# Performance work log

Measured on AMD Instinct MI355X. Metric: run time of the kernel, lower is better.

The kernel has to match this reference:

```python
import jax, jax.numpy as jnp
import numpy as np

N, D, B = 500000, 128, 2048

def setup_inputs() -> dict:
    key = jax.random.key(0)
    ks = jax.random.split(key, 7)
    x = jax.random.normal(ks[0], (N, D), dtype=jnp.float32)
    batch = jnp.sort(jax.random.randint(ks[1], (N,), 0, B)).astype(jnp.int64)
    s = 1.0 / np.sqrt(D)
    Wm = jax.random.uniform(ks[2], (D, D), jnp.float32, -s, s)  # xavier-ish
    fc1_w = jax.random.uniform(ks[3], (D // 4, D), jnp.float32, -s, s)
    fc1_b = jnp.zeros((D // 4,), jnp.float32)
    fc2_w = jax.random.uniform(ks[4], (D, D // 4), jnp.float32, -1/np.sqrt(D//4), 1/np.sqrt(D//4))
    fc2_b = jnp.zeros((D,), jnp.float32)
    return {"x": x, "batch": batch, "size": B, "Wm": Wm,
            "fc1_w": fc1_w, "fc1_b": fc1_b, "fc2_w": fc2_w, "fc2_b": fc2_b}

def reference(x, batch, size, Wm, fc1_w, fc1_b, fc2_w, fc2_b):
    batch = batch.astype(jnp.int32)
    # fc: Linear -> ReLU -> Linear -> Tanh
    attention = jnp.tanh(jax.nn.relu(x @ fc1_w.T + fc1_b) @ fc2_w.T + fc2_b)
    x2 = attention * x + x  # [N, D]
    # scatter_mean over graphs
    sums = jax.ops.segment_sum(x2, batch, num_segments=size)  # [B, D]
    cnt = jax.ops.segment_sum(jnp.ones((x2.shape[0],), x2.dtype), batch, num_segments=size)
    mean = sums / jnp.maximum(cnt, 1.0)[:, None]
    transformed_global = jnp.tanh(mean @ Wm)  # [B, D]
    coefs = jax.nn.sigmoid(jnp.sum(x2 * transformed_global[batch], axis=1))  # [N]
    weighted = coefs[:, None] * x2
    return jax.ops.segment_sum(weighted, batch, num_segments=size)  # [B, D]
```

## Files before the change

### kernel.cpp

```cpp
#include <hip/hip_runtime.h>
#include <math.h>

#define D 128
#define BLOCKS_A 768
#define BLOCKS_C 1536
#define THREADS 256

typedef short s8v __attribute__((ext_vector_type(8)));
typedef float f4v __attribute__((ext_vector_type(4)));

__device__ __forceinline__ float fast_tanh(float z) {
    float e = __expf(2.f * z);
    return 1.f - 2.f / (e + 1.f);
}
__device__ __forceinline__ unsigned cvt_pk_bf16(float lo, float hi) {
    unsigned r;
    asm("v_cvt_pk_bf16_f32 %0, %1, %2" : "=v"(r) : "v"(lo), "v"(hi));
    return r;
}
__device__ __forceinline__ s8v pack8(float4 w0, float4 w1) {
    union { unsigned u[4]; s8v v; } r;
    r.u[0] = cvt_pk_bf16(w0.x, w0.y);
    r.u[1] = cvt_pk_bf16(w0.z, w0.w);
    r.u[2] = cvt_pk_bf16(w1.x, w1.y);
    r.u[3] = cvt_pk_bf16(w1.z, w1.w);
    return r.v;
}

#define EPI0(RG_)                                                             \
    {                                                                         \
        int r = R + quad * 4 + RG_;                                           \
        int seg = batch[r];                                                   \
        const float* xrow = x + (size_t)r * 128 + m15;                        \
        float yv[8];                                                          \
        _Pragma("unroll")                                                     \
        for (int t = 0; t < 8; ++t) {                                         \
            float z = af[t][RG_] + b2l[t];                                    \
            yv[t] = xrow[16 * t] * (1.f + fast_tanh(z));                      \
        }                                                                     \
        union { unsigned u[4]; uint4 q; } pk;                                 \
        pk.u[0] = cvt_pk_bf16(yv[0], yv[1]);                                  \
        pk.u[1] = cvt_pk_bf16(yv[2], yv[3]);                                  \
        pk.u[2] = cvt_pk_bf16(yv[4], yv[5]);                                  \
        pk.u[3] = cvt_pk_bf16(yv[6], yv[7]);                                  \
        ((uint4*)x2s)[(size_t)b * 256 + RG_ * 64 + lane] = pk.q;              \
        if (seg != cur) {                                                     \
            if (cur >= 0) {                                                   \
                _Pragma("unroll")                                             \
                for (int t = 0; t < 8; ++t)                                   \
                    atomicAdd(&sums[cur * 128 + m15 + 16 * t], acc[t]);       \
                if (m15 == 0) atomicAdd(&cnt[cur], acnt);                     \
            }                                                                 \
            cur = seg;                                                        \
            _Pragma("unroll")                                                 \
            for (int t = 0; t < 8; ++t) acc[t] = yv[t];                       \
            acnt = 1.f;                                                       \
        } else {                                                              \
            _Pragma("unroll")                                                 \
            for (int t = 0; t < 8; ++t) acc[t] += yv[t];                      \
            acnt += 1.f;                                                      \
        }                                                                     \
    }

__global__ __launch_bounds__(THREADS, 3) void phaseA(
    const float* __restrict__ x, const int* __restrict__ batch,
    const float* __restrict__ fc1_w, const float* __restrict__ fc1_b,
    const float* __restrict__ fc2_w, const float* __restrict__ fc2_b,
    float* __restrict__ sums, float* __restrict__ cnt,
    unsigned short* __restrict__ x2s, int N)
{
    __shared__ s8v wB1[2][4][64];
    __shared__ s8v wB2[8][64];
    __shared__ float hbuf[4][16 * 36];

    const int lane = threadIdx.x & 63;
    const int wv = threadIdx.x >> 6;
    const int m15 = lane & 15;
    const int quad = lane >> 4;

    if (wv == 0) {
        #pragma unroll
        for (int t = 0; t < 2; ++t)
            #pragma unroll
            for (int kc = 0; kc < 4; ++kc) {
                const float* p = fc1_w + (16 * t + m15) * 128 + kc * 32 + quad * 8;
                wB1[t][kc][lane] = pack8(*(const float4*)p, *(const float4*)(p + 4));
            }
        #pragma unroll
        for (int t = 0; t < 8; ++t) {
            const float* p = fc2_w + (16 * t + m15) * 32 + quad * 8;
            wB2[t][lane] = pack8(*(const float4*)p, *(const float4*)(p + 4));
        }
    }
    float b1l[2], b2l[8];
    #pragma unroll
    for (int t = 0; t < 2; ++t) b1l[t] = fc1_b[m15 + 16 * t];
    #pragma unroll
    for (int t = 0; t < 8; ++t) b2l[t] = fc2_b[m15 + 16 * t];
    __syncthreads();

    const int total16 = N >> 4;
    const int nw = BLOCKS_A * 4;
    const int gw = blockIdx.x * 4 + wv;
    const int base = total16 / nw, rem = total16 % nw;
    const int b0 = gw * base + (gw < rem ? gw : rem);
    const int b1e = b0 + base + (gw < rem ? 1 : 0);

    float* hw = hbuf[wv];

    float acc[8];
    #pragma unroll
    for (int t = 0; t < 8; ++t) acc[t] = 0.f;
    int cur = -1;
    float acnt = 0.f;
    const f4v z4 = {0.f, 0.f, 0.f, 0.f};

    float4 F[8];
    if (b0 < b1e) {
        const float* xp = x + (size_t)(b0 << 4) * D + m15 * 128 + quad * 8;
        #pragma unroll
        for (int kc = 0; kc < 4; ++kc) {
            F[2 * kc]     = *(const float4*)(xp + kc * 32);
            F[2 * kc + 1] = *(const float4*)(xp + kc * 32 + 4);
        }
    }

    for (int b = b0; b < b1e; ++b) {
        const int R = b << 4;
        s8v ax[4];
        #pragma unroll
        for (int kc = 0; kc < 4; ++kc)
            ax[kc] = pack8(F[2 * kc], F[2 * kc + 1]);
        if (b + 1 < b1e) {
            const float* xp = x + (size_t)((b + 1) << 4) * D + m15 * 128 + quad * 8;
            #pragma unroll
            for (int kc = 0; kc < 4; ++kc) {
                F[2 * kc]     = *(const float4*)(xp + kc * 32);
                F[2 * kc + 1] = *(const float4*)(xp + kc * 32 + 4);
            }
        }
        f4v accH[2];
        accH[0] = z4; accH[1] = z4;
        #pragma unroll
        for (int kc = 0; kc < 4; ++kc) {
            accH[0] = __builtin_amdgcn_mfma_f32_16x16x32_bf16(ax[kc], wB1[0][kc][lane], accH[0], 0, 0, 0);
            accH[1] = __builtin_amdgcn_mfma_f32_16x16x32_bf16(ax[kc], wB1[1][kc][lane], accH[1], 0, 0, 0);
        }
        #pragma unroll
        for (int t = 0; t < 2; ++t)
            #pragma unroll
            for (int rg = 0; rg < 4; ++rg) {
                float hv = fmaxf(accH[t][rg] + b1l[t], 0.f);
                hw[(quad * 4 + rg) * 36 + m15 + 16 * t] = hv;
            }
        const f4v h0 = *(const f4v*)&hw[m15 * 36 + quad * 8];
        const f4v h1 = *(const f4v*)&hw[m15 * 36 + quad * 8 + 4];
        union { unsigned u[4]; s8v v; } ahu;
        ahu.u[0] = cvt_pk_bf16(h0[0], h0[1]);
        ahu.u[1] = cvt_pk_bf16(h0[2], h0[3]);
        ahu.u[2] = cvt_pk_bf16(h1[0], h1[1]);
        ahu.u[3] = cvt_pk_bf16(h1[2], h1[3]);
        s8v ah = ahu.v;
        f4v af[8];
        #pragma unroll
        for (int t = 0; t < 8; ++t)
            af[t] = __builtin_amdgcn_mfma_f32_16x16x32_bf16(ah, wB2[t][lane], z4, 0, 0, 0);

        EPI0(0) EPI0(1) EPI0(2) EPI0(3)
    }
    if (cur >= 0) {
        #pragma unroll
        for (int t = 0; t < 8; ++t)
            atomicAdd(&sums[cur * 128 + m15 + 16 * t], acc[t]);
        if (m15 == 0) atomicAdd(&cnt[cur], acnt);
    }
}

__global__ __launch_bounds__(D, 8) void phaseB(
    const float* __restrict__ sums, const float* __restrict__ cnt,
    const float* __restrict__ Wm, float* __restrict__ tg)
{
    int b = blockIdx.x;
    int d = threadIdx.x;
    __shared__ float m[D];
    float inv = 1.f / fmaxf(cnt[b], 1.f);
    m[d] = sums[(b << 7) + d] * inv;
    __syncthreads();
    float acc = 0.f;
    #pragma unroll 8
    for (int k = 0; k < D; ++k)
        acc = fmaf(m[k], Wm[(k << 7) + d], acc);
    tg[(b << 7) + d] = fast_tanh(acc);
}

__global__ __launch_bounds__(THREADS, 6) void phaseC(
    const unsigned short* __restrict__ x2s, const int* __restrict__ batch,
    const float* __restrict__ tg, float* __restrict__ out, int N)
{
    const int lane = threadIdx.x & 63;
    const int wv = threadIdx.x >> 6;
    const int m15 = lane & 15;
    const int quad = lane >> 4;

    const int total16 = N >> 4;
    const int nw = BLOCKS_C * 4;
    const int gw = blockIdx.x * 4 + wv;
    const int base = total16 / nw, rem = total16 % nw;
    const int b0 = gw * base + (gw < rem ? gw : rem);
    const int b1e = b0 + base + (gw < rem ? 1 : 0);

    float acc[8], tgv[8];
    #pragma unroll
    for (int t = 0; t < 8; ++t) { acc[t] = 0.f; tgv[t] = 0.f; }
    int cur = -1;

    for (int b = b0; b < b1e; ++b) {
        const int R = b << 4;
        const uint4* p = (const uint4*)x2s + (size_t)b * 256 + lane;
        uint4 C0 = p[0], C1 = p[64], C2 = p[128], C3 = p[192];
        int sg0 = batch[R + quad * 4 + 0];
        int sg1 = batch[R + quad * 4 + 1];
        int sg2 = batch[R + quad * 4 + 2];
        int sg3 = batch[R + quad * 4 + 3];
        #pragma unroll
        for (int rg = 0; rg < 4; ++rg) {
            uint4 C = rg == 0 ? C0 : rg == 1 ? C1 : rg == 2 ? C2 : C3;
            int seg = rg == 0 ? sg0 : rg == 1 ? sg1 : rg == 2 ? sg2 : sg3;
            if (seg != cur) {
                if (cur >= 0) {
                    #pragma unroll
                    for (int t = 0; t < 8; ++t)
                        atomicAdd(&out[cur * 128 + m15 + 16 * t], acc[t]);
                }
                cur = seg;
                #pragma unroll
                for (int t = 0; t < 8; ++t) {
                    tgv[t] = tg[seg * 128 + m15 + 16 * t];
                    acc[t] = 0.f;
                }
            }
            float xv[8];
            unsigned w;
            union { unsigned u; float f; } cv;
            w = C.x; cv.u = w << 16; xv[0] = cv.f; cv.u = w & 0xffff0000u; xv[1] = cv.f;
            w = C.y; cv.u = w << 16; xv[2] = cv.f; cv.u = w & 0xffff0000u; xv[3] = cv.f;
            w = C.z; cv.u = w << 16; xv[4] = cv.f; cv.u = w & 0xffff0000u; xv[5] = cv.f;
            w = C.w; cv.u = w << 16; xv[6] = cv.f; cv.u = w & 0xffff0000u; xv[7] = cv.f;
            float dot = 0.f;
            #pragma unroll
            for (int t = 0; t < 8; ++t) dot = fmaf(xv[t], tgv[t], dot);
            dot += __shfl_xor(dot, 1);
            dot += __shfl_xor(dot, 2);
            dot += __shfl_xor(dot, 4);
            dot += __shfl_xor(dot, 8);
            float coef = 1.f / (1.f + __expf(-dot));
            #pragma unroll
            for (int t = 0; t < 8; ++t) acc[t] = fmaf(coef, xv[t], acc[t]);
        }
    }
    if (cur >= 0) {
        #pragma unroll
        for (int t = 0; t < 8; ++t)
            atomicAdd(&out[cur * 128 + m15 + 16 * t], acc[t]);
    }
}

extern "C" void kernel_launch(void* const* d_in, const int* in_sizes, int n_in,
                              void* d_out, int out_size, void* d_ws, size_t ws_size,
                              hipStream_t stream) {
    const float* x     = (const float*)d_in[0];
    const int*   batch = (const int*)d_in[1];
    const float* Wm    = (const float*)d_in[3];
    const float* fc1_w = (const float*)d_in[4];
    const float* fc1_b = (const float*)d_in[5];
    const float* fc2_w = (const float*)d_in[6];
    const float* fc2_b = (const float*)d_in[7];
    float* out = (float*)d_out;

    int N = in_sizes[0] / D;
    int B = out_size / D;

    float* sums = (float*)d_ws;
    float* cnt  = sums + (size_t)B * D;
    float* tg   = cnt + B;
    unsigned short* x2s = (unsigned short*)(tg + (size_t)B * D);

    hipMemsetAsync(d_ws, 0, ((size_t)B * D + B) * sizeof(float), stream);
    hipMemsetAsync(d_out, 0, (size_t)out_size * sizeof(float), stream);

    phaseA<<<BLOCKS_A, THREADS, 0, stream>>>(
        x, batch, fc1_w, fc1_b, fc2_w, fc2_b, sums, cnt, x2s, N);
    phaseB<<<B, D, 0, stream>>>(sums, cnt, Wm, tg);
    phaseC<<<BLOCKS_C, THREADS, 0, stream>>>(x2s, batch, tg, out, N);
}
```

Before: 475.1 us.

## Reduce segment atomics via cross-quad shuffle reduction and binary-search counts

Per-16-row tile, rows are bucketed into the first and last segment of the tile. Partial sums are reduced across the four quads with xor shuffles before a single set of atomics per segment, in place of per-lane atomics from every quad. Segment counts are no longer accumulated atomically; phaseB derives them by binary searching the sorted batch array. phaseC occupancy hint lowers from 6 to 4 waves, and rare middle segments fall back to direct atomics.

```diff
diff --git a/kernel.cpp b/kernel.cpp
--- a/kernel.cpp
+++ b/kernel.cpp
@@ -26,6 +26,19 @@
     r.u[3] = cvt_pk_bf16(w1.z, w1.w);
     return r.v;
 }
+
+#define RFLUSH(ACC_, SEG_, DST_)                                              \
+    if ((SEG_) >= 0) {                                                        \
+        _Pragma("unroll")                                                     \
+        for (int t = 0; t < 8; ++t) {                                         \
+            ACC_[t] += __shfl_xor(ACC_[t], 16);                               \
+            ACC_[t] += __shfl_xor(ACC_[t], 32);                               \
+        }                                                                     \
+        _Pragma("unroll")                                                     \
+        for (int t = 0; t < 8; ++t)                                           \
+            if ((t >> 1) == quad)                                             \
+                atomicAdd(&(DST_)[(size_t)(SEG_) * 128 + m15 + 16 * t], ACC_[t]); \
+    }
 
 #define EPI0(RG_)                                                             \
     {                                                                         \
@@ -44,21 +57,16 @@
         pk.u[2] = cvt_pk_bf16(yv[4], yv[5]);                                  \
         pk.u[3] = cvt_pk_bf16(yv[6], yv[7]);                                  \
         ((uint4*)x2s)[(size_t)b * 256 + RG_ * 64 + lane] = pk.q;              \
-        if (seg != cur) {                                                     \
-            if (cur >= 0) {                                                   \
-                _Pragma("unroll")                                             \
-                for (int t = 0; t < 8; ++t)                                   \
-                    atomicAdd(&sums[cur * 128 + m15 + 16 * t], acc[t]);       \
-                if (m15 == 0) atomicAdd(&cnt[cur], acnt);                     \
-            }                                                                 \
-            cur = seg;                                                        \
+        if (seg == segLo) {                                                   \
             _Pragma("unroll")                                                 \
-            for (int t = 0; t < 8; ++t) acc[t] = yv[t];                       \
-            acnt = 1.f;                                                       \
+            for (int t = 0; t < 8; ++t) tl[t] += yv[t];                       \
+        } else if (seg == segHi) {                                            \
+            _Pragma("unroll")                                                 \
+            for (int t = 0; t < 8; ++t) th[t] += yv[t];                       \
         } else {                                                              \
             _Pragma("unroll")                                                 \
-            for (int t = 0; t < 8; ++t) acc[t] += yv[t];                      \
-            acnt += 1.f;                                                      \
+            for (int t = 0; t < 8; ++t)                                       \
+                atomicAdd(&sums[(size_t)seg * 128 + m15 + 16 * t], yv[t]);    \
         }                                                                     \
     }
 
@@ -66,8 +74,7 @@
     const float* __restrict__ x, const int* __restrict__ batch,
     const float* __restrict__ fc1_w, const float* __restrict__ fc1_b,
     const float* __restrict__ fc2_w, const float* __restrict__ fc2_b,
-    float* __restrict__ sums, float* __restrict__ cnt,
-    unsigned short* __restrict__ x2s, int N)
+    float* __restrict__ sums, unsigned short* __restrict__ x2s, int N)
 {
     __shared__ s8v wB1[2][4][64];
     __shared__ s8v wB2[8][64];
@@ -108,11 +115,10 @@
 
     float* hw = hbuf[wv];
 
-    float acc[8];
+    float accW[8];
     #pragma unroll
-    for (int t = 0; t < 8; ++t) acc[t] = 0.f;
-    int cur = -1;
-    float acnt = 0.f;
+    for (int t = 0; t < 8; ++t) accW[t] = 0.f;
+    int curW = -1;
     const f4v z4 = {0.f, 0.f, 0.f, 0.f};
 
     float4 F[8];
@@ -166,24 +172,52 @@
         for (int t = 0; t < 8; ++t)
             af[t] = __builtin_amdgcn_mfma_f32_16x16x32_bf16(ah, wB2[t][lane], z4, 0, 0, 0);
 
+        const int segLo = batch[R];
+        const int segHi = batch[R + 15];
+        float tl[8], th[8];
+        #pragma unroll
+        for (int t = 0; t < 8; ++t) { tl[t] = 0.f; th[t] = 0.f; }
+
         EPI0(0) EPI0(1) EPI0(2) EPI0(3)
-    }
-    if (cur >= 0) {
-        #pragma unroll
-        for (int t = 0; t < 8; ++t)
-            atomicAdd(&sums[cur * 128 + m15 + 16 * t], acc[t]);
-        if (m15 == 0) atomicAdd(&cnt[cur], acnt);
-    }
+
+        if (segLo == curW) {
+            #pragma unroll
+            for (int t = 0; t < 8; ++t) accW[t] += tl[t];
+        } else {
+            RFLUSH(accW, curW, sums)
+            curW = segLo;
+            #pragma unroll
+            for (int t = 0; t < 8; ++t) accW[t] = tl[t];
+        }
+        if (segHi != segLo) {
+            RFLUSH(accW, curW, sums)
+            curW = segHi;
+            #pragma unroll
+            for (int t = 0; t < 8; ++t) accW[t] = th[t];
+        }
+    }
+    RFLUSH(accW, curW, sums)
 }
 
 __global__ __launch_bounds__(D, 8) void phaseB(
-    const float* __restrict__ sums, const float* __restrict__ cnt,
-    const float* __restrict__ Wm, float* __restrict__ tg)
+    const float* __restrict__ sums, const int* __restrict__ batch,
+    const float* __restrict__ Wm, float* __restrict__ tg, int N)
 {
     int b = blockIdx.x;
     int d = threadIdx.x;
     __shared__ float m[D];
-    float inv = 1.f / fmaxf(cnt[b], 1.f);
+    __shared__ int bnd[2];
+    if (d < 2) {
+        int target = b + d;
+        int lo = 0, hi = N;
+        while (lo < hi) {
+            int mid = (lo + hi) >> 1;
+            if (batch[mid] < target) lo = mid + 1; else hi = mid;
+        }
+        bnd[d] = lo;
+    }
+    __syncthreads();
+    float inv = 1.f / fmaxf((float)(bnd[1] - bnd[0]), 1.f);
     m[d] = sums[(b << 7) + d] * inv;
     __syncthreads();
     float acc = 0.f;
@@ -193,7 +227,14 @@
     tg[(b << 7) + d] = fast_tanh(acc);
 }
 
-__global__ __launch_bounds__(THREADS, 6) void phaseC(
+__device__ __forceinline__ float bf_lo(unsigned w) {
+    union { unsigned u; float f; } v; v.u = w << 16; return v.f;
+}
+__device__ __forceinline__ float bf_hi(unsigned w) {
+    union { unsigned u; float f; } v; v.u = w & 0xffff0000u; return v.f;
+}
+
+__global__ __launch_bounds__(THREADS, 4) void phaseC(
     const unsigned short* __restrict__ x2s, const int* __restrict__ batch,
     const float* __restrict__ tg, float* __restrict__ out, int N)
 {
@@ -209,43 +250,37 @@
     const int b0 = gw * base + (gw < rem ? gw : rem);
     const int b1e = b0 + base + (gw < rem ? 1 : 0);
 
-    float acc[8], tgv[8];
+    float accW[8], tgv[8];
     #pragma unroll
-    for (int t = 0; t < 8; ++t) { acc[t] = 0.f; tgv[t] = 0.f; }
-    int cur = -1;
+    for (int t = 0; t < 8; ++t) { accW[t] = 0.f; tgv[t] = 0.f; }
+    int curW = -1;
+    int curT = -1;
 
     for (int b = b0; b < b1e; ++b) {
         const int R = b << 4;
         const uint4* p = (const uint4*)x2s + (size_t)b * 256 + lane;
         uint4 C0 = p[0], C1 = p[64], C2 = p[128], C3 = p[192];
-        int sg0 = batch[R + quad * 4 + 0];
-        int sg1 = batch[R + quad * 4 + 1];
-        int sg2 = batch[R + quad * 4 + 2];
-        int sg3 = batch[R + quad * 4 + 3];
+        const int segLo = batch[R];
+        const int segHi = batch[R + 15];
+        float tl[8], th[8];
+        #pragma unroll
+        for (int t = 0; t < 8; ++t) { tl[t] = 0.f; th[t] = 0.f; }
+
         #pragma unroll
         for (int rg = 0; rg < 4; ++rg) {
             uint4 C = rg == 0 ? C0 : rg == 1 ? C1 : rg == 2 ? C2 : C3;
-            int seg = rg == 0 ? sg0 : rg == 1 ? sg1 : rg == 2 ? sg2 : sg3;
-            if (seg != cur) {
-                if (cur >= 0) {
-                    #pragma unroll
-                    for (int t = 0; t < 8; ++t)
-                        atomicAdd(&out[cur * 128 + m15 + 16 * t], acc[t]);
-                }
-                cur = seg;
+            int seg = batch[R + quad * 4 + rg];
+            if (seg != curT) {
+                curT = seg;
                 #pragma unroll
-                for (int t = 0; t < 8; ++t) {
-                    tgv[t] = tg[seg * 128 + m15 + 16 * t];
-                    acc[t] = 0.f;
-                }
+                for (int t = 0; t < 8; ++t)
+                    tgv[t] = tg[(size_t)seg * 128 + m15 + 16 * t];
             }
             float xv[8];
-            unsigned w;
-            union { unsigned u; float f; } cv;
-            w = C.x; cv.u = w << 16; xv[0] = cv.f; cv.u = w & 0xffff0000u; xv[1] = cv.f;
-            w = C.y; cv.u = w << 16; xv[2] = cv.f; cv.u = w & 0xffff0000u; xv[3] = cv.f;
-            w = C.z; cv.u = w << 16; xv[4] = cv.f; cv.u = w & 0xffff0000u; xv[5] = cv.f;
-            w = C.w; cv.u = w << 16; xv[6] = cv.f; cv.u = w & 0xffff0000u; xv[7] = cv.f;
+            xv[0] = bf_lo(C.x); xv[1] = bf_hi(C.x);
+            xv[2] = bf_lo(C.y); xv[3] = bf_hi(C.y);
+            xv[4] = bf_lo(C.z); xv[5] = bf_hi(C.z);
+            xv[6] = bf_lo(C.w); xv[7] = bf_hi(C.w);
             float dot = 0.f;
             #pragma unroll
             for (int t = 0; t < 8; ++t) dot = fmaf(xv[t], tgv[t], dot);
@@ -254,15 +289,36 @@
             dot += __shfl_xor(dot, 4);
             dot += __shfl_xor(dot, 8);
             float coef = 1.f / (1.f + __expf(-dot));
-            #pragma unroll
-            for (int t = 0; t < 8; ++t) acc[t] = fmaf(coef, xv[t], acc[t]);
-        }
-    }
-    if (cur >= 0) {
-        #pragma unroll
-        for (int t = 0; t < 8; ++t)
-            atomicAdd(&out[cur * 128 + m15 + 16 * t], acc[t]);
-    }
+            if (seg == segLo) {
+                #pragma unroll
+                for (int t = 0; t < 8; ++t) tl[t] = fmaf(coef, xv[t], tl[t]);
+            } else if (seg == segHi) {
+                #pragma unroll
+                for (int t = 0; t < 8; ++t) th[t] = fmaf(coef, xv[t], th[t]);
+            } else {
+                #pragma unroll
+                for (int t = 0; t < 8; ++t)
+                    atomicAdd(&out[(size_t)seg * 128 + m15 + 16 * t], coef * xv[t]);
+            }
+        }
+
+        if (segLo == curW) {
+            #pragma unroll
+            for (int t = 0; t < 8; ++t) accW[t] += tl[t];
+        } else {
+            RFLUSH(accW, curW, out)
+            curW = segLo;
+            #pragma unroll
+            for (int t = 0; t < 8; ++t) accW[t] = tl[t];
+        }
+        if (segHi != segLo) {
+            RFLUSH(accW, curW, out)
+            curW = segHi;
+            #pragma unroll
+            for (int t = 0; t < 8; ++t) accW[t] = th[t];
+        }
+    }
+    RFLUSH(accW, curW, out)
 }
 
 extern "C" void kernel_launch(void* const* d_in, const int* in_sizes, int n_in,
@@ -281,15 +337,14 @@
     int B = out_size / D;
 
     float* sums = (float*)d_ws;
-    float* cnt  = sums + (size_t)B * D;
-    float* tg   = cnt + B;
+    float* tg   = sums + (size_t)B * D;
     unsigned short* x2s = (unsigned short*)(tg + (size_t)B * D);
 
-    hipMemsetAsync(d_ws, 0, ((size_t)B * D + B) * sizeof(float), stream);
+    hipMemsetAsync(d_ws, 0, (size_t)B * D * sizeof(float), stream);
     hipMemsetAsync(d_out, 0, (size_t)out_size * sizeof(float), stream);
 
     phaseA<<<BLOCKS_A, THREADS, 0, stream>>>(
-        x, batch, fc1_w, fc1_b, fc2_w, fc2_b, sums, cnt, x2s, N);
-    phaseB<<<B, D, 0, stream>>>(sums, cnt, Wm, tg);
+        x, batch, fc1_w, fc1_b, fc2_w, fc2_b, sums, x2s, N);
+    phaseB<<<B, D, 0, stream>>>(sums, batch, Wm, tg, N);
     phaseC<<<BLOCKS_C, THREADS, 0, stream>>>(x2s, batch, tg, out, N);
 }
```

After: 447.7 us. 5.8% less time.
